# Performance work log

Measured on AMD Instinct MI355X. Metric: run time of the kernel, lower is better.

Reference implementation:

```python
import jax, jax.numpy as jnp
import numpy as np

TEMPERATURE = 0.5
EPS = 1e-8  # matches torchmetrics' safe-norm clamp


def setup_inputs() -> dict:
    key = jax.random.key(0)
    x = jax.random.normal(key, (16384, 512), dtype=jnp.float32)
    return {"x": x}


def reference(x):
    # pairwise_cosine_similarity(x) (torchmetrics): sim = n @ n.T with n = x/||x||,
    # diagonal zeroed by default (zero_diagonal=True when y is None).
    norm = jnp.maximum(jnp.linalg.norm(x, axis=-1, keepdims=True), EPS)
    n = x / norm                                   # [N, D] L2-normalized
    sim = jnp.einsum('nd,md->nm', n, n)            # [N, N] cosine similarity
    diag = jnp.einsum('nd,nd->n', n, n)            # ||n_i||^2 == sim diagonal
    row_sum = sim.sum(-1) - diag                   # zero_diagonal=True
    return (row_sum / TEMPERATURE).mean()
```

## Files before the change

kernel.cpp:

```cpp
#include <hip/hip_runtime.h>

#define DIM 512
#define TEMPERATURE 0.5f
#define EPS 1e-8f

__global__ void init_ws_kernel(float* __restrict__ ws) {
    int t = threadIdx.x;
    if (t < DIM + 1) ws[t] = 0.0f;
}

__global__ __launch_bounds__(256) void accum_kernel(const float* __restrict__ x,
                                                    float* __restrict__ ws, int N) {
    const int tid  = threadIdx.x;
    const int wave = tid >> 6;
    const int lane = tid & 63;
    const int rowBase = blockIdx.x * 64;

    float4 accA = make_float4(0.f, 0.f, 0.f, 0.f);
    float4 accB = make_float4(0.f, 0.f, 0.f, 0.f);
    float diag_acc = 0.f;

    for (int r = wave; r < 64; r += 4) {
        const int row = rowBase + r;
        if (row >= N) break;
        const float4* p = (const float4*)(x + (size_t)row * DIM);
        float4 a = p[lane];
        float4 b = p[lane + 64];

        float ss = a.x * a.x + a.y * a.y + a.z * a.z + a.w * a.w
                 + b.x * b.x + b.y * b.y + b.z * b.z + b.w * b.w;
        #pragma unroll
        for (int off = 1; off < 64; off <<= 1)
            ss += __shfl_xor(ss, off);

        const float inv = 1.0f / fmaxf(sqrtf(ss), EPS);
        if (lane == 0) diag_acc += ss * inv * inv;

        accA.x += a.x * inv; accA.y += a.y * inv; accA.z += a.z * inv; accA.w += a.w * inv;
        accB.x += b.x * inv; accB.y += b.y * inv; accB.z += b.z * inv; accB.w += b.w * inv;
    }

    __shared__ float sred[4][DIM];
    __shared__ float dred[4];
    float* myrow = sred[wave];
    myrow[lane * 4 + 0] = accA.x;
    myrow[lane * 4 + 1] = accA.y;
    myrow[lane * 4 + 2] = accA.z;
    myrow[lane * 4 + 3] = accA.w;
    myrow[256 + lane * 4 + 0] = accB.x;
    myrow[256 + lane * 4 + 1] = accB.y;
    myrow[256 + lane * 4 + 2] = accB.z;
    myrow[256 + lane * 4 + 3] = accB.w;
    if (lane == 0) dred[wave] = diag_acc;
    __syncthreads();

    #pragma unroll
    for (int idx = tid; idx < DIM; idx += 256) {
        float v = sred[0][idx] + sred[1][idx] + sred[2][idx] + sred[3][idx];
        atomicAdd(&ws[idx], v);
    }
    if (tid == 0) atomicAdd(&ws[DIM], dred[0] + dred[1] + dred[2] + dred[3]);
}

__global__ __launch_bounds__(256) void finalize_kernel(const float* __restrict__ ws,
                                                       float* __restrict__ out, int N) {
    const int tid = threadIdx.x;
    const float v0 = ws[tid];
    const float v1 = ws[tid + 256];
    float ss = v0 * v0 + v1 * v1;
    #pragma unroll
    for (int off = 1; off < 64; off <<= 1)
        ss += __shfl_xor(ss, off);

    __shared__ float wred[4];
    if ((tid & 63) == 0) wred[tid >> 6] = ss;
    __syncthreads();
    if (tid == 0) {
        const float total = wred[0] + wred[1] + wred[2] + wred[3];
        out[0] = (total - ws[DIM]) / (TEMPERATURE * (float)N);
    }
}

extern "C" void kernel_launch(void* const* d_in, const int* in_sizes, int n_in,
                              void* d_out, int out_size, void* d_ws, size_t ws_size,
                              hipStream_t stream) {
    const float* x = (const float*)d_in[0];
    float* ws = (float*)d_ws;
    float* out = (float*)d_out;
    const int N = in_sizes[0] / DIM;

    init_ws_kernel<<<1, 576, 0, stream>>>(ws);
    const int blocks = (N + 63) / 64;
    accum_kernel<<<blocks, 256, 0, stream>>>(x, ws, N);
    finalize_kernel<<<1, 256, 0, stream>>>(ws, out, N);
}
```

Before: 84.84 us.

## Replace global atomics with per-block partials and drop init kernel

Each block now writes its 512-column partial sum and diagonal term to its own slot instead of doing atomicAdds on a shared workspace. This removes the zero-init kernel launch and atomic contention. Blocks grow to 512 threads (8 waves, 8 rows each), and the full-tile path is unrolled with FMAs. The finalize kernel now serially sums 256 partial rows per column in a single block, which adds a small serial tail.

```diff
diff --git a/kernel.cpp b/kernel.cpp
--- a/kernel.cpp
+++ b/kernel.cpp
@@ -1,83 +1,100 @@
 #include <hip/hip_runtime.h>
 
 #define DIM 512
-#define TEMPERATURE 0.5f
+#define TEMP 0.5f
 #define EPS 1e-8f
+#define BT 512
+#define ROWS_PER_BLK 64
+#define PSTRIDE (DIM + 1)
 
-__global__ void init_ws_kernel(float* __restrict__ ws) {
-    int t = threadIdx.x;
-    if (t < DIM + 1) ws[t] = 0.0f;
-}
-
-__global__ __launch_bounds__(256) void accum_kernel(const float* __restrict__ x,
-                                                    float* __restrict__ ws, int N) {
+__global__ __launch_bounds__(BT) void accum_kernel(const float* __restrict__ x,
+                                                   float* __restrict__ part, int N) {
     const int tid  = threadIdx.x;
     const int wave = tid >> 6;
     const int lane = tid & 63;
-    const int rowBase = blockIdx.x * 64;
+    const int rowBase = blockIdx.x * ROWS_PER_BLK;
 
     float4 accA = make_float4(0.f, 0.f, 0.f, 0.f);
     float4 accB = make_float4(0.f, 0.f, 0.f, 0.f);
-    float diag_acc = 0.f;
+    float diag = 0.f;
 
-    for (int r = wave; r < 64; r += 4) {
-        const int row = rowBase + r;
-        if (row >= N) break;
-        const float4* p = (const float4*)(x + (size_t)row * DIM);
-        float4 a = p[lane];
-        float4 b = p[lane + 64];
-
-        float ss = a.x * a.x + a.y * a.y + a.z * a.z + a.w * a.w
-                 + b.x * b.x + b.y * b.y + b.z * b.z + b.w * b.w;
+    if (rowBase + ROWS_PER_BLK <= N) {
         #pragma unroll
-        for (int off = 1; off < 64; off <<= 1)
-            ss += __shfl_xor(ss, off);
-
-        const float inv = 1.0f / fmaxf(sqrtf(ss), EPS);
-        if (lane == 0) diag_acc += ss * inv * inv;
-
-        accA.x += a.x * inv; accA.y += a.y * inv; accA.z += a.z * inv; accA.w += a.w * inv;
-        accB.x += b.x * inv; accB.y += b.y * inv; accB.z += b.z * inv; accB.w += b.w * inv;
+        for (int rr = 0; rr < 8; ++rr) {
+            const int row = rowBase + wave + rr * 8;
+            const float4* p = (const float4*)(x + (size_t)row * DIM);
+            const float4 a = p[lane];
+            const float4 b = p[lane + 64];
+            float ss = a.x * a.x + a.y * a.y + a.z * a.z + a.w * a.w
+                     + b.x * b.x + b.y * b.y + b.z * b.z + b.w * b.w;
+            #pragma unroll
+            for (int off = 1; off < 64; off <<= 1) ss += __shfl_xor(ss, off);
+            const float inv = 1.0f / fmaxf(sqrtf(ss), EPS);
+            if (lane == 0) diag += ss * inv * inv;
+            accA.x = fmaf(a.x, inv, accA.x); accA.y = fmaf(a.y, inv, accA.y);
+            accA.z = fmaf(a.z, inv, accA.z); accA.w = fmaf(a.w, inv, accA.w);
+            accB.x = fmaf(b.x, inv, accB.x); accB.y = fmaf(b.y, inv, accB.y);
+            accB.z = fmaf(b.z, inv, accB.z); accB.w = fmaf(b.w, inv, accB.w);
+        }
+    } else {
+        for (int rr = 0; rr < 8; ++rr) {
+            const int row = rowBase + wave + rr * 8;
+            if (row >= N) break;
+            const float4* p = (const float4*)(x + (size_t)row * DIM);
+            const float4 a = p[lane];
+            const float4 b = p[lane + 64];
+            float ss = a.x * a.x + a.y * a.y + a.z * a.z + a.w * a.w
+                     + b.x * b.x + b.y * b.y + b.z * b.z + b.w * b.w;
+            #pragma unroll
+            for (int off = 1; off < 64; off <<= 1) ss += __shfl_xor(ss, off);
+            const float inv = 1.0f / fmaxf(sqrtf(ss), EPS);
+            if (lane == 0) diag += ss * inv * inv;
+            accA.x = fmaf(a.x, inv, accA.x); accA.y = fmaf(a.y, inv, accA.y);
+            accA.z = fmaf(a.z, inv, accA.z); accA.w = fmaf(a.w, inv, accA.w);
+            accB.x = fmaf(b.x, inv, accB.x); accB.y = fmaf(b.y, inv, accB.y);
+            accB.z = fmaf(b.z, inv, accB.z); accB.w = fmaf(b.w, inv, accB.w);
+        }
     }
 
-    __shared__ float sred[4][DIM];
-    __shared__ float dred[4];
-    float* myrow = sred[wave];
-    myrow[lane * 4 + 0] = accA.x;
-    myrow[lane * 4 + 1] = accA.y;
-    myrow[lane * 4 + 2] = accA.z;
-    myrow[lane * 4 + 3] = accA.w;
-    myrow[256 + lane * 4 + 0] = accB.x;
-    myrow[256 + lane * 4 + 1] = accB.y;
-    myrow[256 + lane * 4 + 2] = accB.z;
-    myrow[256 + lane * 4 + 3] = accB.w;
-    if (lane == 0) dred[wave] = diag_acc;
+    __shared__ float sred[8][DIM];
+    __shared__ float dred[8];
+    *(float4*)&sred[wave][lane * 4]       = accA;
+    *(float4*)&sred[wave][256 + lane * 4] = accB;
+    if (lane == 0) dred[wave] = diag;
     __syncthreads();
 
+    float v = 0.f;
     #pragma unroll
-    for (int idx = tid; idx < DIM; idx += 256) {
-        float v = sred[0][idx] + sred[1][idx] + sred[2][idx] + sred[3][idx];
-        atomicAdd(&ws[idx], v);
+    for (int w = 0; w < 8; ++w) v += sred[w][tid];
+    part[(size_t)blockIdx.x * PSTRIDE + tid] = v;
+    if (tid == 0) {
+        float d = 0.f;
+        #pragma unroll
+        for (int w = 0; w < 8; ++w) d += dred[w];
+        part[(size_t)blockIdx.x * PSTRIDE + DIM] = d;
     }
-    if (tid == 0) atomicAdd(&ws[DIM], dred[0] + dred[1] + dred[2] + dred[3]);
 }
 
-__global__ __launch_bounds__(256) void finalize_kernel(const float* __restrict__ ws,
-                                                       float* __restrict__ out, int N) {
-    const int tid = threadIdx.x;
-    const float v0 = ws[tid];
-    const float v1 = ws[tid + 256];
-    float ss = v0 * v0 + v1 * v1;
+__global__ __launch_bounds__(BT) void finalize_kernel(const float* __restrict__ part,
+                                                      float* __restrict__ out,
+                                                      int nblk, int N) {
+    const int t = threadIdx.x;
+    float acc = 0.f;
+    #pragma unroll 8
+    for (int b = 0; b < nblk; ++b) acc += part[(size_t)b * PSTRIDE + t];
+    float v = acc * acc;
+    if (t < nblk) v -= part[(size_t)t * PSTRIDE + DIM];
     #pragma unroll
-    for (int off = 1; off < 64; off <<= 1)
-        ss += __shfl_xor(ss, off);
+    for (int off = 1; off < 64; off <<= 1) v += __shfl_xor(v, off);
 
-    __shared__ float wred[4];
-    if ((tid & 63) == 0) wred[tid >> 6] = ss;
+    __shared__ float wred[8];
+    if ((t & 63) == 0) wred[t >> 6] = v;
     __syncthreads();
-    if (tid == 0) {
-        const float total = wred[0] + wred[1] + wred[2] + wred[3];
-        out[0] = (total - ws[DIM]) / (TEMPERATURE * (float)N);
+    if (t == 0) {
+        float tot = 0.f;
+        #pragma unroll
+        for (int w = 0; w < 8; ++w) tot += wred[w];
+        out[0] = tot / (TEMP * (float)N);
     }
 }
 
@@ -85,12 +102,11 @@
                               void* d_out, int out_size, void* d_ws, size_t ws_size,
                               hipStream_t stream) {
     const float* x = (const float*)d_in[0];
-    float* ws = (float*)d_ws;
+    float* part = (float*)d_ws;
     float* out = (float*)d_out;
     const int N = in_sizes[0] / DIM;
+    const int nblk = (N + ROWS_PER_BLK - 1) / ROWS_PER_BLK;
 
-    init_ws_kernel<<<1, 576, 0, stream>>>(ws);
-    const int blocks = (N + 63) / 64;
-    accum_kernel<<<blocks, 256, 0, stream>>>(x, ws, N);
-    finalize_kernel<<<1, 256, 0, stream>>>(ws, out, N);
+    accum_kernel<<<nblk, BT, 0, stream>>>(x, part, N);
+    finalize_kernel<<<1, BT, 0, stream>>>(part, out, nblk, N);
 }
```

Result: slower. 91.34 us (+7.7%).
